# Kernel tuning notes

Hardware: AMD Instinct MI355X
Metric: run time of the kernel (lower is better)

## Reference

```python
import jax, jax.numpy as jnp
import numpy as np

# Dimensions (ModelNet40-style point-cloud classification)
B, N, KNN, T = 4, 1024, 20, 10
BETA, LAM, EPS = 1.0, 1.0, 1e-6
TAU, TH_POS, TH_NEG = 20.0, 1.0, -1.0
NUM_CLASSES = 40


@jax.custom_vjp
def spike(x):
    # Heaviside with fast-sigmoid surrogate gradient (standard SNN practice)
    return (x >= 0).astype(x.dtype)

def _spike_fwd(x):
    return (x >= 0).astype(x.dtype), x

def _spike_bwd(x, g):
    return (g / (1.0 + jnp.abs(x)) ** 2,)

spike.defvjp(_spike_fwd, _spike_bwd)


def setup_inputs() -> dict:
    key = jax.random.key(0)
    ks = jax.random.split(key, 8)

    def lin(k, fin, fout):
        return jax.random.normal(k, (fin, fout), jnp.float32) / float(np.sqrt(fin))

    def cheb(k, fin, fout):  # [K=3, F_in, F_out] Chebyshev filter bank
        return jax.random.normal(k, (3, fin, fout), jnp.float32) / float(np.sqrt(fin))

    return {
        "point_cloud": jax.random.normal(ks[0], (B, N, 3), jnp.float32),
        "enc_W": lin(ks[1], 3, 64), "enc_b": jnp.zeros((64,), jnp.float32),
        "W0": cheb(ks[2], 64, 64), "b0": jnp.zeros((64,), jnp.float32),
        "W1": cheb(ks[3], 128, 128), "b1": jnp.zeros((128,), jnp.float32),
        "W2": cheb(ks[4], 256, 256), "b2": jnp.zeros((256,), jnp.float32),
        "ro_W": lin(ks[5], 512, NUM_CLASSES), "ro_b": jnp.zeros((NUM_CLASSES,), jnp.float32),
    }


def build_graph(pc):
    # Local-density-adaptive kNN graph: [B,N,KNN] neighbor idx, edge weights, per-node scale
    d2 = jnp.sum((pc[:, :, None, :] - pc[:, None, :, :]) ** 2, -1)  # [B,N,N]
    d2 = d2 + jnp.eye(pc.shape[1], dtype=pc.dtype) * 1e9            # exclude self
    negv, idx = jax.lax.top_k(-d2, KNN)
    dist = jnp.sqrt(jnp.maximum(-negv, 1e-12))                      # [B,N,KNN]
    sigma = BETA * jnp.mean(dist, -1) + EPS                         # adaptive sigma [B,N]
    w = jnp.exp(-dist ** 2 / sigma[..., None] ** 2)
    w = w / (jnp.sum(w, -1, keepdims=True) + EPS)                   # row-normalized
    return idx, w, LAM * sigma                                      # s_local = lambda*sigma


def lap_apply(x, idx, w, s):
    # Node-adaptive scaled Laplacian: s_i * (x_i - sum_j w_ij x_j); x: [B,T,N,F]
    neigh = jax.vmap(lambda xb, ib: xb[:, ib])(x, idx)              # [B,T,N,KNN,F]
    agg = jnp.einsum('bnk,btnkf->btnf', w, neigh)
    return s[:, None, :, None] * (x - agg)


def wavelet_conv(x, idx, w, s, Wc, bc):
    # Chebyshev order-3 graph wavelet conv: T0=x, T1=Lx, T2=2L(T1)-T0
    t1 = lap_apply(x, idx, w, s)
    t2 = 2.0 * lap_apply(t1, idx, w, s) - x
    return jnp.einsum('kbtnf,kfg->btng', jnp.stack([x, t1, t2]), Wc) + bc


def bipolar_lif(x):
    # Bipolar LIF with dual thresholds; soft reset; output concat([pos, neg]) doubles F
    decay = jnp.exp(jnp.asarray(-1.0 / TAU, x.dtype))
    def step(v, xt):
        v = decay * v + xt
        sp = spike(v - TH_POS)
        sn = spike(TH_NEG - v)
        v = v - sp * TH_POS - sn * TH_NEG
        return v, jnp.concatenate([sp, sn], -1)
    v0 = jnp.zeros((x.shape[0],) + x.shape[2:], x.dtype)
    _, out = jax.lax.scan(step, v0, jnp.swapaxes(x, 0, 1))          # scan over T
    return jnp.swapaxes(out, 0, 1)                                  # [B,T,N,2F]


def reference(point_cloud, enc_W, enc_b, W0, b0, W1, b1, W2, b2, ro_W, ro_b):
    idx, w, s = build_graph(point_cloud)
    feat = jax.nn.relu(point_cloud @ enc_W + enc_b)                 # [B,N,64]
    rates = jnp.clip(feat, 0.0, 1.0)
    u = jax.random.uniform(jax.random.key(42), (feat.shape[0], T) + feat.shape[1:], feat.dtype)
    spikes = (u < rates[:, None]).astype(feat.dtype)                # Poisson rate encoding [B,T,N,64]
    for Wc, bc in ((W0, b0), (W1, b1), (W2, b2)):
        spikes = bipolar_lif(wavelet_conv(spikes, idx, w, s, Wc, bc))
    rate = jnp.mean(spikes, axis=1)                                 # rate readout over time
    pooled = jnp.mean(rate, axis=1)                                 # global average pool over nodes
    return pooled @ ro_W + ro_b                                     # [B, NUM_CLASSES]
```

## Files before the change

### kernel.cpp

```cpp
#include <hip/hip_runtime.h>
#include <stdint.h>
#include <math.h>

#pragma clang fp contract(off)

#define NB 4
#define NN 1024
#define KNN 20
#define NT 10

__global__ __launch_bounds__(256) void graph_kernel(const float* __restrict__ pc,
        int* __restrict__ idx_out, float* __restrict__ w_out, float* __restrict__ s_out){
  int row = blockIdx.x;
  int b = row >> 10, i = row & (NN-1);
  int tid = threadIdx.x;
  __shared__ float d2s[NN];
  __shared__ unsigned long long red[256];
  __shared__ int   sel_idx[KNN];
  __shared__ float sel_d2[KNN];
  const float* pb = pc + (size_t)b*NN*3;
  float xi = pb[i*3+0], yi = pb[i*3+1], zi = pb[i*3+2];
  for (int j=tid; j<NN; j+=256){
    float dx = xi - pb[j*3+0];
    float dy = yi - pb[j*3+1];
    float dz = zi - pb[j*3+2];
    float d2 = dx*dx;
    d2 = d2 + dy*dy;
    d2 = d2 + dz*dz;
    if (j==i) d2 = d2 + 1e9f;
    d2s[j] = d2;
  }
  __syncthreads();
  for (int k=0;k<KNN;k++){
    unsigned long long best = 0xffffffffffffffffull;
    for (int j=tid;j<NN;j+=256){
      unsigned long long key = ((unsigned long long)__float_as_uint(d2s[j])<<32) | (unsigned int)j;
      if (key < best) best = key;
    }
    red[tid] = best;
    __syncthreads();
    for (int off=128; off>0; off>>=1){
      if (tid < off){ if (red[tid+off] < red[tid]) red[tid] = red[tid+off]; }
      __syncthreads();
    }
    if (tid==0){
      unsigned long long bk = red[0];
      int bj = (int)(bk & 0xffffffffu);
      sel_idx[k] = bj;
      sel_d2[k]  = __uint_as_float((unsigned int)(bk >> 32));
      d2s[bj] = __uint_as_float(0x7f800000u);
    }
    __syncthreads();
  }
  if (tid==0){
    float dist[KNN]; float dsum = 0.0f;
    for (int k=0;k<KNN;k++){ dist[k] = sqrtf(fmaxf(sel_d2[k], 1e-12f)); dsum = dsum + dist[k]; }
    float sigma = dsum / 20.0f;
    sigma = 1.0f * sigma + 1e-6f;
    float s2 = sigma * sigma;
    float wv[KNN]; float wsum = 0.0f;
    for (int k=0;k<KNN;k++){
      float ds = dist[k]*dist[k];
      wv[k] = expf((-ds)/s2);
      wsum = wsum + wv[k];
    }
    float denom = wsum + 1e-6f;
    for (int k=0;k<KNN;k++){
      w_out[(size_t)row*KNN+k]  = wv[k] / denom;
      idx_out[(size_t)row*KNN+k] = sel_idx[k];
    }
    s_out[row] = 1.0f * sigma;
  }
}

__global__ void enc_kernel(const float* __restrict__ pc, const float* __restrict__ W,
                           const float* __restrict__ bias, float* __restrict__ rates){
  int id = blockIdx.x*blockDim.x + threadIdx.x;
  if (id >= NB*NN*64) return;
  int f = id & 63; int bn = id >> 6;
  float p0 = pc[bn*3+0], p1 = pc[bn*3+1], p2 = pc[bn*3+2];
  float acc = fmaf(p0, W[0*64+f], 0.0f);
  acc = fmaf(p1, W[1*64+f], acc);
  acc = fmaf(p2, W[2*64+f], acc);
  acc = acc + bias[f];
  acc = fmaxf(acc, 0.0f);
  acc = fminf(fmaxf(acc, 0.0f), 1.0f);
  rates[id] = acc;
}

__device__ __forceinline__ uint32_t rotl32(uint32_t x, uint32_t r){ return (x<<r) | (x>>(32u-r)); }

__global__ void poisson_kernel(const float* __restrict__ rates, uint8_t* __restrict__ out){
  const uint32_t H = (uint32_t)(NB*NT*NN*64) / 2u;
  uint32_t i = blockIdx.x*blockDim.x + threadIdx.x;
  if (i >= H) return;
  const uint32_t ks0 = 0u, ks1 = 42u;
  const uint32_t ks2 = ks0 ^ ks1 ^ 0x1BD11BDAu;
  uint32_t x0 = i + ks0;
  uint32_t x1 = (i + H) + ks1;
#define TF4(a,b,c,d) \
  x0 += x1; x1 = rotl32(x1,a); x1 ^= x0; \
  x0 += x1; x1 = rotl32(x1,b); x1 ^= x0; \
  x0 += x1; x1 = rotl32(x1,c); x1 ^= x0; \
  x0 += x1; x1 = rotl32(x1,d); x1 ^= x0;
  TF4(13u,15u,26u,6u)  x0 += ks1; x1 += ks2 + 1u;
  TF4(17u,29u,16u,24u) x0 += ks2; x1 += ks0 + 2u;
  TF4(13u,15u,26u,6u)  x0 += ks0; x1 += ks1 + 3u;
  TF4(17u,29u,16u,24u) x0 += ks1; x1 += ks2 + 4u;
  TF4(13u,15u,26u,6u)  x0 += ks2; x1 += ks0 + 5u;
#undef TF4
  {
    uint32_t m = i;
    float u = __uint_as_float((x0 >> 9) | 0x3f800000u) - 1.0f;
    uint32_t f = m & 63u, n = (m >> 6) & (NN-1);
    uint32_t bt = m >> 16; uint32_t b = bt / NT;
    float rate = rates[(((size_t)b<<10) + n)*64 + f];
    out[m] = (u < rate) ? (uint8_t)1 : (uint8_t)0;
  }
  {
    uint32_t m = i + H;
    float u = __uint_as_float((x1 >> 9) | 0x3f800000u) - 1.0f;
    uint32_t f = m & 63u, n = (m >> 6) & (NN-1);
    uint32_t bt = m >> 16; uint32_t b = bt / NT;
    float rate = rates[(((size_t)b<<10) + n)*64 + f];
    out[m] = (u < rate) ? (uint8_t)1 : (uint8_t)0;
  }
}

template<int F>
__global__ __launch_bounds__(256) void lap1_kernel3(const uint8_t* __restrict__ x,
        const int* __restrict__ idx, const float* __restrict__ w, const float* __restrict__ s,
        float* __restrict__ t1, int t0){
  constexpr int TPN = F / 4;
  constexpr int R   = 256 / TPN;
  int tid = threadIdx.x;
  int rsub = tid / TPN;
  int f4 = tid % TPN;
  int row = blockIdx.x * R + rsub;
  int bn = row % (NB*NN); int tt = row / (NB*NN);
  int b = bn >> 10; int n = bn & (NN-1); int t = t0 + tt;
  __shared__ int   nidx[R][KNN];
  __shared__ float nw[R][KNN];
  __shared__ float sv[R];
  int bn0 = (blockIdx.x * R) % (NB*NN);
  for (int e=tid; e<R*KNN; e+=256){
    int r = e / KNN, k = e % KNN;
    nidx[r][k] = idx[(size_t)(bn0+r)*KNN+k];
    nw[r][k]   = w[(size_t)(bn0+r)*KNN+k];
  }
  for (int e=tid; e<R; e+=256) sv[e] = s[bn0+e];
  __syncthreads();
  const uint8_t* xb = x + ((size_t)(b*NT + t)*NN)*F;
  float a0=0.f,a1=0.f,a2=0.f,a3=0.f;
  for (int k=0;k<KNN;k++){
    float wk = nw[rsub][k];
    uchar4 u = *(const uchar4*)(xb + (size_t)nidx[rsub][k]*F + f4*4);
    a0 = fmaf(wk, (float)u.x, a0);
    a1 = fmaf(wk, (float)u.y, a1);
    a2 = fmaf(wk, (float)u.z, a2);
    a3 = fmaf(wk, (float)u.w, a3);
  }
  uchar4 ux = *(const uchar4*)(xb + (size_t)n*F + f4*4);
  float sl = sv[rsub];
  float4 o;
  o.x = sl * ((float)ux.x - a0);
  o.y = sl * ((float)ux.y - a1);
  o.z = sl * ((float)ux.z - a2);
  o.w = sl * ((float)ux.w - a3);
  *(float4*)(t1 + (size_t)row*F + f4*4) = o;
}

template<int F>
__global__ __launch_bounds__(256) void lap2_kernel3(const uint8_t* __restrict__ x,
        const float* __restrict__ t1, const int* __restrict__ idx, const float* __restrict__ w,
        const float* __restrict__ s, float* __restrict__ t2, int t0){
  constexpr int TPN = F / 4;
  constexpr int R   = 256 / TPN;
  int tid = threadIdx.x;
  int rsub = tid / TPN;
  int f4 = tid % TPN;
  int row = blockIdx.x * R + rsub;
  int bn = row % (NB*NN); int tt = row / (NB*NN);
  int b = bn >> 10; int n = bn & (NN-1); int t = t0 + tt;
  __shared__ int   nidx[R][KNN];
  __shared__ float nw[R][KNN];
  __shared__ float sv[R];
  int bn0 = (blockIdx.x * R) % (NB*NN);
  for (int e=tid; e<R*KNN; e+=256){
    int r = e / KNN, k = e % KNN;
    nidx[r][k] = idx[(size_t)(bn0+r)*KNN+k];
    nw[r][k]   = w[(size_t)(bn0+r)*KNN+k];
  }
  for (int e=tid; e<R; e+=256) sv[e] = s[bn0+e];
  __syncthreads();
  const float* t1b = t1 + ((size_t)tt*(NB*NN) + (size_t)b*NN)*F;
  float a0=0.f,a1=0.f,a2=0.f,a3=0.f;
  for (int k=0;k<KNN;k++){
    float wk = nw[rsub][k];
    float4 v = *(const float4*)(t1b + (size_t)nidx[rsub][k]*F + f4*4);
    a0 = fmaf(wk, v.x, a0);
    a1 = fmaf(wk, v.y, a1);
    a2 = fmaf(wk, v.z, a2);
    a3 = fmaf(wk, v.w, a3);
  }
  float4 tv = *(const float4*)(t1 + (size_t)row*F + f4*4);
  uchar4 ux = *(const uchar4*)(x + ((size_t)(b*NT + t)*NN + n)*F + f4*4);
  float sl = sv[rsub];
  float4 o;
  o.x = 2.0f * (sl * (tv.x - a0)) - (float)ux.x;
  o.y = 2.0f * (sl * (tv.y - a1)) - (float)ux.y;
  o.z = 2.0f * (sl * (tv.z - a2)) - (float)ux.z;
  o.w = 2.0f * (sl * (tv.w - a3)) - (float)ux.w;
  *(float4*)(t2 + (size_t)row*F + f4*4) = o;
}

template<int F, int G, int BN, int TN>
__global__ __launch_bounds__(256) void conv_gemm3_kernel(const uint8_t* __restrict__ x,
        const float* __restrict__ t1, const float* __restrict__ t2,
        const float* __restrict__ W, float* __restrict__ abuf, int t0){
  constexpr int BM = 64, BK = 16, TM = 4;
  constexpr int NTX = BN / TN;
  constexpr int NTY = 256 / NTX;
  static_assert(NTY * TM == BM, "tile mismatch");
  constexpr int LDA = BM + 4;
  constexpr int LDB = BN + 4;
  __shared__ float As[BK * LDA];
  __shared__ float Ws[BK * LDB];

  const int tid = threadIdx.x;
  const int tx = tid % NTX, ty = tid / NTX;
  const int row0 = blockIdx.x * BM;
  const int g0 = blockIdx.y * BN;

  const int arow = tid >> 2;
  const int akg  = (tid & 3) * 4;
  const int grow = row0 + arow;
  const int bn_a = grow % (NB*NN);
  const int tt_a = grow / (NB*NN);
  const int b_a = bn_a >> 10, n_a = bn_a & (NN-1);
  const uint8_t* xrow  = x  + ((size_t)(b_a*NT + t0 + tt_a)*NN + n_a)*F;
  const float*   t1row = t1 + (size_t)grow * F;
  const float*   t2row = t2 + (size_t)grow * F;

  float acc[TM][TN];
  #pragma unroll
  for (int r=0;r<TM;r++)
    #pragma unroll
    for (int c=0;c<TN;c++) acc[r][c] = 0.0f;

  for (int s = 0; s < 3; ++s){
    for (int f0 = 0; f0 < F; f0 += BK){
      if (s == 0){
        uchar4 u = *(const uchar4*)(xrow + f0 + akg);
        As[(akg+0)*LDA + arow] = (float)u.x;
        As[(akg+1)*LDA + arow] = (float)u.y;
        As[(akg+2)*LDA + arow] = (float)u.z;
        As[(akg+3)*LDA + arow] = (float)u.w;
      } else {
        const float* src = ((s==1) ? t1row : t2row) + f0 + akg;
        float4 v = *(const float4*)src;
        As[(akg+0)*LDA + arow] = v.x;
        As[(akg+1)*LDA + arow] = v.y;
        As[(akg+2)*LDA + arow] = v.z;
        As[(akg+3)*LDA + arow] = v.w;
      }
      const float* Wsrc = W + ((size_t)(s*F + f0))*G + g0;
      #pragma unroll
      for (int e = 0; e < (BK*BN)/(256*4); ++e){
        int idx2 = tid + e*256;
        int wk = idx2 / (BN/4);
        int wg = (idx2 % (BN/4))*4;
        *(float4*)&Ws[wk*LDB + wg] = *(const float4*)(Wsrc + (size_t)wk*G + wg);
      }
      __syncthreads();
      #pragma unroll
      for (int k = 0; k < BK; ++k){
        float a[TM];
        *(float2*)&a[0] = *(const float2*)&As[k*LDA + ty*2];
        *(float2*)&a[2] = *(const float2*)&As[k*LDA + BM/2 + ty*2];
        float wv[TN];
        if constexpr (TN == 8){
          *(float4*)&wv[0] = *(const float4*)&Ws[k*LDB + tx*4];
          *(float4*)&wv[4] = *(const float4*)&Ws[k*LDB + BN/2 + tx*4];
        } else {
          *(float2*)&wv[0] = *(const float2*)&Ws[k*LDB + tx*2];
          *(float2*)&wv[2] = *(const float2*)&Ws[k*LDB + BN/2 + tx*2];
        }
        #pragma unroll
        for (int r=0;r<TM;r++)
          #pragma unroll
          for (int c=0;c<TN;c++)
            acc[r][c] = fmaf(a[r], wv[c], acc[r][c]);
      }
      __syncthreads();
    }
  }
  #pragma unroll
  for (int rg=0; rg<2; ++rg){
    #pragma unroll
    for (int r=0; r<TM/2; ++r){
      float* dst = abuf + (size_t)(row0 + rg*(BM/2) + ty*2 + r)*G + g0;
      if constexpr (TN == 8){
        *(float4*)(dst + tx*4)        = *(float4*)&acc[rg*2+r][0];
        *(float4*)(dst + BN/2 + tx*4) = *(float4*)&acc[rg*2+r][4];
      } else {
        *(float2*)(dst + tx*2)        = *(float2*)&acc[rg*2+r][0];
        *(float2*)(dst + BN/2 + tx*2) = *(float2*)&acc[rg*2+r][2];
      }
    }
  }
}

__global__ void lif_kernel(const float* __restrict__ abuf, const float* __restrict__ bias,
        float* __restrict__ vbuf, uint8_t* __restrict__ out, int t0, int tc, int G, float decay){
  int id = blockIdx.x*blockDim.x + threadIdx.x;
  if (id >= NB*NN*G) return;
  int g = id % G;
  int bn = id / G;
  int b = bn >> 10, n = bn & (NN-1);
  float v = (t0 == 0) ? 0.0f : vbuf[id];
  float bg = bias[g];
  for (int tt=0; tt<tc; ++tt){
    float a = abuf[((size_t)tt*(NB*NN) + bn)*G + g] + bg;
    float vn = decay * v + a;
    float sp  = ((vn - 1.0f) >= 0.0f) ? 1.0f : 0.0f;
    float snk = ((-1.0f - vn) >= 0.0f) ? 1.0f : 0.0f;
    vn = vn - sp * 1.0f;
    vn = vn - snk * (-1.0f);
    v = vn;
    uint8_t* ob = out + ((size_t)(b*NT + t0 + tt)*NN + n)*((size_t)2*G);
    ob[g]   = (uint8_t)sp;
    ob[G+g] = (uint8_t)snk;
  }
  if (t0 + tc < NT) vbuf[id] = v;
}

__global__ void pool_partial_kernel(const uint8_t* __restrict__ sp, uint32_t* __restrict__ partial){
  int b = blockIdx.x >> 6;
  int chunk = blockIdx.x & 63;
  int n0 = chunk * 16;
  int u = threadIdx.x;
  uint32_t c0=0,c1=0,c2=0,c3=0;
  for (int t=0;t<NT;t++){
    for (int n=0;n<16;n++){
      const uint32_t* rowp = (const uint32_t*)(sp + ((size_t)(b*NT+t)*NN + n0+n)*512);
      uint32_t wv = rowp[u];
      c0 += wv & 0xffu;
      c1 += (wv >> 8) & 0xffu;
      c2 += (wv >> 16) & 0xffu;
      c3 += wv >> 24;
    }
  }
  uint32_t* op = partial + (size_t)blockIdx.x*512 + u*4;
  op[0]=c0; op[1]=c1; op[2]=c2; op[3]=c3;
}

__global__ __launch_bounds__(512) void finalize_head_kernel(const uint32_t* __restrict__ partial,
        const float* __restrict__ roW, const float* __restrict__ rob, float* __restrict__ out){
  int b = blockIdx.x;
  int f = threadIdx.x;
  __shared__ float pooled[512];
  uint32_t cnt = 0;
  for (int ch=0; ch<64; ch++)
    cnt += partial[((size_t)(b*64+ch))*512 + f];
  pooled[f] = (float)cnt / 10.0f / 1024.0f;
  __syncthreads();
  if (f < 40){
    float acc = 0.0f;
    for (int k=0;k<512;k++)
      acc = fmaf(pooled[k], roW[k*40+f], acc);
    out[b*40 + f] = acc + rob[f];
  }
}

extern "C" void kernel_launch(void* const* d_in, const int* in_sizes, int n_in,
                              void* d_out, int out_size, void* d_ws, size_t ws_size,
                              hipStream_t stream) {
  const float* pc   = (const float*)d_in[0];
  const float* encW = (const float*)d_in[1];
  const float* encB = (const float*)d_in[2];
  const float* W0   = (const float*)d_in[3];
  const float* b0   = (const float*)d_in[4];
  const float* W1   = (const float*)d_in[5];
  const float* b1   = (const float*)d_in[6];
  const float* W2   = (const float*)d_in[7];
  const float* b2   = (const float*)d_in[8];
  const float* roW  = (const float*)d_in[9];
  const float* rob  = (const float*)d_in[10];
  float* outp = (float*)d_out;

  char* p = (char*)d_ws;
  auto alloc = [&](size_t bytes)->char*{
    char* r = p; p += (bytes + 255) & ~(size_t)255; return r;
  };
  int*      idxb   = (int*)     alloc((size_t)NB*NN*KNN*4);
  float*    wb     = (float*)   alloc((size_t)NB*NN*KNN*4);
  float*    sb     = (float*)   alloc((size_t)NB*NN*4);
  float*    rates  = (float*)   alloc((size_t)NB*NN*64*4);
  float*    vbuf   = (float*)   alloc((size_t)NB*NN*256*4);
  uint32_t* partial= (uint32_t*)alloc((size_t)NB*64*512*4);
  uint8_t*  bufA   = (uint8_t*) alloc((size_t)NB*NT*NN*512);
  uint8_t*  bufB   = (uint8_t*) alloc((size_t)NB*NT*NN*512);

  size_t used = (size_t)(p - (char*)d_ws);
  size_t per_t = (size_t)NB*NN*256*4*3;
  int TC = 1;
  if (ws_size > used + per_t){
    size_t tcc = (ws_size - used) / per_t;
    TC = (tcc >= NT) ? NT : (int)tcc;
    if (TC < 1) TC = 1;
  }
  float* t1b  = (float*)alloc((size_t)NB*(size_t)TC*NN*256*4);
  float* t2b  = (float*)alloc((size_t)NB*(size_t)TC*NN*256*4);
  float* abuf = (float*)alloc((size_t)NB*(size_t)TC*NN*256*4);

  graph_kernel<<<NB*NN, 256, 0, stream>>>(pc, idxb, wb, sb);
  enc_kernel<<<(NB*NN*64 + 255)/256, 256, 0, stream>>>(pc, encW, encB, rates);
  {
    const uint32_t H = (uint32_t)(NB*NT*NN*64) / 2u;
    poisson_kernel<<<(H + 255)/256, 256, 0, stream>>>(rates, bufA);
  }

  float decay = expf(-1.0f / 20.0f);

  uint8_t* xin  = bufA;
  uint8_t* xout = bufB;
  for (int l=0; l<3; l++){
    int G = (l==0)?64:(l==1)?128:256;
    const float* Wc = (l==0)?W0:(l==1)?W1:W2;
    const float* bc = (l==0)?b0:(l==1)?b1:b2;
    for (int t0=0; t0<NT; t0+=TC){
      int tc = (NT - t0 < TC) ? (NT - t0) : TC;
      int M = NB*NN*tc;
      if (l==0){
        lap1_kernel3<64><<<M/16, 256, 0, stream>>>(xin, idxb, wb, sb, t1b, t0);
        lap2_kernel3<64><<<M/16, 256, 0, stream>>>(xin, t1b, idxb, wb, sb, t2b, t0);
        dim3 grid(M/64, 1);
        conv_gemm3_kernel<64,64,64,4><<<grid, 256, 0, stream>>>(xin, t1b, t2b, Wc, abuf, t0);
      } else if (l==1){
        lap1_kernel3<128><<<M/8, 256, 0, stream>>>(xin, idxb, wb, sb, t1b, t0);
        lap2_kernel3<128><<<M/8, 256, 0, stream>>>(xin, t1b, idxb, wb, sb, t2b, t0);
        dim3 grid(M/64, 2);
        conv_gemm3_kernel<128,128,64,4><<<grid, 256, 0, stream>>>(xin, t1b, t2b, Wc, abuf, t0);
      } else {
        lap1_kernel3<256><<<M/4, 256, 0, stream>>>(xin, idxb, wb, sb, t1b, t0);
        lap2_kernel3<256><<<M/4, 256, 0, stream>>>(xin, t1b, idxb, wb, sb, t2b, t0);
        dim3 grid(M/64, 2);
        conv_gemm3_kernel<256,256,128,8><<<grid, 256, 0, stream>>>(xin, t1b, t2b, Wc, abuf, t0);
      }
      lif_kernel<<<(NB*NN*G + 255)/256, 256, 0, stream>>>(abuf, bc, vbuf, xout, t0, tc, G, decay);
    }
    uint8_t* tmp = xin; xin = xout; xout = tmp;
  }

  pool_partial_kernel<<<NB*64, 128, 0, stream>>>(xin, partial);
  finalize_head_kernel<<<NB, 512, 0, stream>>>(partial, roW, rob, outp);
}
```

Measured before the change: 532.1 us.

## Prefetch GEMM tiles into registers and use wave-shuffle reduction in kNN selection

The conv GEMM now loads the next K-tile of activations and weights into registers while computing on the current shared-memory tile. This software pipeline is meant to hide global-memory latency behind the FMA loop, at the cost of extra registers per thread. Separately, the kNN argmin reduction replaces an 8-step shared-memory tree, which synchronised after every step, with 64-lane wave shuffles plus a 4-way final compare. That cuts barriers in each of the 20 selection iterations.

```diff
diff --git a/kernel.cpp b/kernel.cpp
--- a/kernel.cpp
+++ b/kernel.cpp
@@ -14,8 +14,9 @@
   int row = blockIdx.x;
   int b = row >> 10, i = row & (NN-1);
   int tid = threadIdx.x;
+  int lane = tid & 63, wid = tid >> 6;
   __shared__ float d2s[NN];
-  __shared__ unsigned long long red[256];
+  __shared__ unsigned long long redw[4];
   __shared__ int   sel_idx[KNN];
   __shared__ float sel_d2[KNN];
   const float* pb = pc + (size_t)b*NN*3;
@@ -37,14 +38,18 @@
       unsigned long long key = ((unsigned long long)__float_as_uint(d2s[j])<<32) | (unsigned int)j;
       if (key < best) best = key;
     }
-    red[tid] = best;
+    #pragma unroll
+    for (int off=32; off>0; off>>=1){
+      unsigned long long o = __shfl_xor(best, off);
+      if (o < best) best = o;
+    }
+    if (lane==0) redw[wid] = best;
     __syncthreads();
-    for (int off=128; off>0; off>>=1){
-      if (tid < off){ if (red[tid+off] < red[tid]) red[tid] = red[tid+off]; }
-      __syncthreads();
-    }
     if (tid==0){
-      unsigned long long bk = red[0];
+      unsigned long long bk = redw[0];
+      if (redw[1] < bk) bk = redw[1];
+      if (redw[2] < bk) bk = redw[2];
+      if (redw[3] < bk) bk = redw[3];
       int bj = (int)(bk & 0xffffffffu);
       sel_idx[k] = bj;
       sel_d2[k]  = __uint_as_float((unsigned int)(bk >> 32));
@@ -215,7 +220,7 @@
 }
 
 template<int F, int G, int BN, int TN>
-__global__ __launch_bounds__(256) void conv_gemm3_kernel(const uint8_t* __restrict__ x,
+__global__ __launch_bounds__(256) void conv_gemm5_kernel(const uint8_t* __restrict__ x,
         const float* __restrict__ t1, const float* __restrict__ t2,
         const float* __restrict__ W, float* __restrict__ abuf, int t0){
   constexpr int BM = 64, BK = 16, TM = 4;
@@ -224,6 +229,8 @@
   static_assert(NTY * TM == BM, "tile mismatch");
   constexpr int LDA = BM + 4;
   constexpr int LDB = BN + 4;
+  constexpr int NTILES = 3 * F / BK;
+  constexpr int WLOADS = (BK*BN)/(256*4);
   __shared__ float As[BK * LDA];
   __shared__ float Ws[BK * LDB];
 
@@ -242,59 +249,86 @@
   const float*   t1row = t1 + (size_t)grow * F;
   const float*   t2row = t2 + (size_t)grow * F;
 
+  int wk[WLOADS], wg[WLOADS];
+  #pragma unroll
+  for (int e=0;e<WLOADS;e++){
+    int idx2 = tid + e*256;
+    wk[e] = idx2 / (BN/4);
+    wg[e] = (idx2 % (BN/4))*4;
+  }
+
+  uint32_t axu;
+  float4   axf;
+  float4   wreg[WLOADS];
+
+  auto load_tile = [&](int tile){
+    int s  = (tile * BK) / F;
+    int f0 = (tile * BK) % F;
+    if (s == 0){
+      axu = *(const uint32_t*)(xrow + f0 + akg);
+    } else {
+      axf = *(const float4*)(((s==1) ? t1row : t2row) + f0 + akg);
+    }
+    const float* Wsrc = W + ((size_t)(s*F + f0))*G + g0;
+    #pragma unroll
+    for (int e=0;e<WLOADS;e++)
+      wreg[e] = *(const float4*)(Wsrc + (size_t)wk[e]*G + wg[e]);
+  };
+  auto store_tile = [&](int tile){
+    int s = (tile * BK) / F;
+    if (s == 0){
+      As[(akg+0)*LDA + arow] = (float)( axu        & 0xffu);
+      As[(akg+1)*LDA + arow] = (float)((axu >> 8)  & 0xffu);
+      As[(akg+2)*LDA + arow] = (float)((axu >> 16) & 0xffu);
+      As[(akg+3)*LDA + arow] = (float)( axu >> 24);
+    } else {
+      As[(akg+0)*LDA + arow] = axf.x;
+      As[(akg+1)*LDA + arow] = axf.y;
+      As[(akg+2)*LDA + arow] = axf.z;
+      As[(akg+3)*LDA + arow] = axf.w;
+    }
+    #pragma unroll
+    for (int e=0;e<WLOADS;e++)
+      *(float4*)&Ws[wk[e]*LDB + wg[e]] = wreg[e];
+  };
+
   float acc[TM][TN];
   #pragma unroll
   for (int r=0;r<TM;r++)
     #pragma unroll
     for (int c=0;c<TN;c++) acc[r][c] = 0.0f;
 
-  for (int s = 0; s < 3; ++s){
-    for (int f0 = 0; f0 < F; f0 += BK){
-      if (s == 0){
-        uchar4 u = *(const uchar4*)(xrow + f0 + akg);
-        As[(akg+0)*LDA + arow] = (float)u.x;
-        As[(akg+1)*LDA + arow] = (float)u.y;
-        As[(akg+2)*LDA + arow] = (float)u.z;
-        As[(akg+3)*LDA + arow] = (float)u.w;
+  auto compute = [&](){
+    #pragma unroll
+    for (int k = 0; k < BK; ++k){
+      float a[TM];
+      *(float2*)&a[0] = *(const float2*)&As[k*LDA + ty*2];
+      *(float2*)&a[2] = *(const float2*)&As[k*LDA + BM/2 + ty*2];
+      float wv[TN];
+      if constexpr (TN == 8){
+        *(float4*)&wv[0] = *(const float4*)&Ws[k*LDB + tx*4];
+        *(float4*)&wv[4] = *(const float4*)&Ws[k*LDB + BN/2 + tx*4];
       } else {
-        const float* src = ((s==1) ? t1row : t2row) + f0 + akg;
-        float4 v = *(const float4*)src;
-        As[(akg+0)*LDA + arow] = v.x;
-        As[(akg+1)*LDA + arow] = v.y;
-        As[(akg+2)*LDA + arow] = v.z;
-        As[(akg+3)*LDA + arow] = v.w;
+        *(float2*)&wv[0] = *(const float2*)&Ws[k*LDB + tx*2];
+        *(float2*)&wv[2] = *(const float2*)&Ws[k*LDB + BN/2 + tx*2];
       }
-      const float* Wsrc = W + ((size_t)(s*F + f0))*G + g0;
       #pragma unroll
-      for (int e = 0; e < (BK*BN)/(256*4); ++e){
-        int idx2 = tid + e*256;
-        int wk = idx2 / (BN/4);
-        int wg = (idx2 % (BN/4))*4;
-        *(float4*)&Ws[wk*LDB + wg] = *(const float4*)(Wsrc + (size_t)wk*G + wg);
-      }
-      __syncthreads();
-      #pragma unroll
-      for (int k = 0; k < BK; ++k){
-        float a[TM];
-        *(float2*)&a[0] = *(const float2*)&As[k*LDA + ty*2];
-        *(float2*)&a[2] = *(const float2*)&As[k*LDA + BM/2 + ty*2];
-        float wv[TN];
-        if constexpr (TN == 8){
-          *(float4*)&wv[0] = *(const float4*)&Ws[k*LDB + tx*4];
-          *(float4*)&wv[4] = *(const float4*)&Ws[k*LDB + BN/2 + tx*4];
-        } else {
-          *(float2*)&wv[0] = *(const float2*)&Ws[k*LDB + tx*2];
-          *(float2*)&wv[2] = *(const float2*)&Ws[k*LDB + BN/2 + tx*2];
-        }
+      for (int r=0;r<TM;r++)
         #pragma unroll
-        for (int r=0;r<TM;r++)
-          #pragma unroll
-          for (int c=0;c<TN;c++)
-            acc[r][c] = fmaf(a[r], wv[c], acc[r][c]);
-      }
-      __syncthreads();
-    }
-  }
+        for (int c=0;c<TN;c++)
+          acc[r][c] = fmaf(a[r], wv[c], acc[r][c]);
+    }
+  };
+
+  load_tile(0);
+  for (int i = 0; i < NTILES; ++i){
+    store_tile(i);
+    __syncthreads();
+    if (i+1 < NTILES) load_tile(i+1);
+    compute();
+    __syncthreads();
+  }
+
   #pragma unroll
   for (int rg=0; rg<2; ++rg){
     #pragma unroll
@@ -436,17 +470,17 @@
         lap1_kernel3<64><<<M/16, 256, 0, stream>>>(xin, idxb, wb, sb, t1b, t0);
         lap2_kernel3<64><<<M/16, 256, 0, stream>>>(xin, t1b, idxb, wb, sb, t2b, t0);
         dim3 grid(M/64, 1);
-        conv_gemm3_kernel<64,64,64,4><<<grid, 256, 0, stream>>>(xin, t1b, t2b, Wc, abuf, t0);
+        conv_gemm5_kernel<64,64,64,4><<<grid, 256, 0, stream>>>(xin, t1b, t2b, Wc, abuf, t0);
       } else if (l==1){
         lap1_kernel3<128><<<M/8, 256, 0, stream>>>(xin, idxb, wb, sb, t1b, t0);
         lap2_kernel3<128><<<M/8, 256, 0, stream>>>(xin, t1b, idxb, wb, sb, t2b, t0);
         dim3 grid(M/64, 2);
-        conv_gemm3_kernel<128,128,64,4><<<grid, 256, 0, stream>>>(xin, t1b, t2b, Wc, abuf, t0);
+        conv_gemm5_kernel<128,128,64,4><<<grid, 256, 0, stream>>>(xin, t1b, t2b, Wc, abuf, t0);
       } else {
         lap1_kernel3<256><<<M/4, 256, 0, stream>>>(xin, idxb, wb, sb, t1b, t0);
         lap2_kernel3<256><<<M/4, 256, 0, stream>>>(xin, t1b, idxb, wb, sb, t2b, t0);
         dim3 grid(M/64, 2);
-        conv_gemm3_kernel<256,256,128,8><<<grid, 256, 0, stream>>>(xin, t1b, t2b, Wc, abuf, t0);
+        conv_gemm5_kernel<256,256,128,8><<<grid, 256, 0, stream>>>(xin, t1b, t2b, Wc, abuf, t0);
       }
       lif_kernel<<<(NB*NN*G + 255)/256, 256, 0, stream>>>(abuf, bc, vbuf, xout, t0, tc, G, decay);
     }
```

Measured after the change: 564.3 us. 1.06x slower.
